# Kernel tuning notes

Measured on AMD Instinct MI355X. Metric: run time of the kernel, lower is better.

Reference implementation:

```python
import jax, jax.numpy as jnp
import numpy as np

N_DIM = 1024
N_HEAD = 16
HEAD_DIM = N_DIM // N_HEAD  # 64
HALF = HEAD_DIM // 2        # 32, per-axis RoPE dim
BASE = 10000.0


def _rope_1d(x, pos, dim_h, base=BASE):
    # x: [B,H,S,dim_h], pos: [B,H,S] int
    theta = 1.0 / (base ** (jnp.arange(0, dim_h, 2, dtype=jnp.float32) / dim_h))  # [dim_h/2]
    pos_c = jnp.maximum(pos, 0)
    ang = pos_c[..., None].astype(jnp.float32) * theta  # [B,H,S,dim_h/2]
    cos, sin = jnp.cos(ang), jnp.sin(ang)
    xs = x.astype(jnp.float32).reshape(*x.shape[:-1], dim_h // 2, 2)
    x0, x1 = xs[..., 0], xs[..., 1]
    r0 = x0 * cos - x1 * sin
    r1 = x1 * cos + x0 * sin
    m = (pos >= 0)[..., None]  # [B,H,S,1]
    r0 = jnp.where(m, r0, x0)
    r1 = jnp.where(m, r1, x1)
    out = jnp.stack([r0, r1], axis=-1).reshape(x.shape)
    return out.astype(x.dtype)


def _rope_2d(x, positions):
    # x: [B,H,S,D], positions: [B,1,S,2] -> expand over heads
    B, H, S, D = x.shape
    pos = jnp.broadcast_to(positions, (B, H, S, 2))
    xh = _rope_1d(x[..., :HALF], pos[..., 0], HALF)
    xw = _rope_1d(x[..., HALF:], pos[..., 1], HALF)
    return jnp.concatenate([xh, xw], axis=-1)


def setup_inputs() -> dict:
    key = jax.random.key(0)
    k1, k2, k3, k4 = jax.random.split(key, 4)
    B, T = 8, 1024
    x = jax.random.normal(k1, (B, T, N_DIM), dtype=jnp.float32)
    attn_mask = jnp.ones((B, 1, T), dtype=bool)
    positions = jax.random.randint(k2, (B, T, 2), 0, 1024, dtype=jnp.int64)
    s = 1.0 / np.sqrt(N_DIM)
    w_qkv = jax.random.normal(k3, (N_DIM, 3 * N_DIM), dtype=jnp.float32) * s
    w_proj = jax.random.normal(k4, (N_DIM, N_DIM), dtype=jnp.float32) * s
    return {"x": x, "attn_mask": attn_mask, "positions": positions,
            "w_qkv": w_qkv, "w_proj": w_proj}


def reference(x, attn_mask, positions, w_qkv, w_proj):
    B, T, C = x.shape
    qkv = x @ w_qkv  # [B,T,3C]
    q, k, v = jnp.split(qkv, 3, axis=2)
    # -> [B,H,T,D]
    def to_heads(t):
        return t.reshape(B, T, N_HEAD, HEAD_DIM).transpose(0, 2, 1, 3)
    q, k, v = to_heads(q), to_heads(k), to_heads(v)
    pos = positions[:, None]  # [B,1,S,2]
    q = _rope_2d(q, pos)
    k = _rope_2d(k, pos)
    scale = 1.0 / np.sqrt(HEAD_DIM)
    scores = jnp.einsum("bhsd,bhtd->bhst", q, k) * scale  # [B,H,T,T]
    mask = attn_mask[:, None]  # [B,1,1,T]
    scores = jnp.where(mask, scores, jnp.float32(-1e30))
    attn = jax.nn.softmax(scores, axis=-1)
    out = jnp.einsum("bhst,bhtd->bhsd", attn, v)  # [B,H,T,D]
    out = out.transpose(0, 2, 1, 3).reshape(B, T, C)
    y = out @ w_proj
    return y
```

## Files before the change

### kernel.cpp

```cpp
#include <hip/hip_runtime.h>
#include <math.h>

#define BATCH 8
#define TSEQ 1024
#define NDIM 1024
#define NHEAD 16
#define HDIM 64
#define QKV_COLS 3072

#define QSCALE 0.18033688011112042f
#define DEFER_THR 10.0f

#define EXP2F(x) __builtin_amdgcn_exp2f(x)

typedef __attribute__((ext_vector_type(8))) short bf16x8;
typedef __attribute__((ext_vector_type(4))) float f32x4;

__device__ inline unsigned short f2bf(float x) {
    unsigned u = __float_as_uint(x);
    unsigned r = u + 0x7fffu + ((u >> 16) & 1u);
    return (unsigned short)(r >> 16);
}
__device__ inline float bf2f(unsigned short h) {
    return __uint_as_float(((unsigned)h) << 16);
}

__device__ inline void gl16(const unsigned short* g, unsigned short* l) {
    __builtin_amdgcn_global_load_lds(
        (const __attribute__((address_space(1))) unsigned int*)g,
        (__attribute__((address_space(3))) unsigned int*)l, 16, 0, 0);
}

template<int OUT_BF16>
__global__ __launch_bounds__(256)
void gemm_bf16k(const unsigned short* __restrict__ A,
                const unsigned short* __restrict__ BT,
                void* __restrict__ Cv, int M, int N, int K) {
    __shared__ unsigned short As[128 * 32];
    __shared__ unsigned short Bs[128 * 32];
    const int tid  = threadIdx.x;
    const int wave = tid >> 6, lane = tid & 63;
    const int row0 = blockIdx.y * 128, col0 = blockIdx.x * 128;
    const int wr = (wave >> 1) * 64, wc = (wave & 1) * 64;

    f32x4 acc[4][4] = {};

    const int srow = lane >> 2;
    const int scol = (lane & 3) * 8;
    const size_t abase = (size_t)row0 * K;
    const size_t bbase = (size_t)col0 * K;
    const int i0 = wave * 2;

    for (int kt = 0; kt < K; kt += 32) {
        __syncthreads();
        gl16(&A [abase + (size_t)(i0 * 16 + srow) * K + kt + scol], &As[i0 * 512]);
        gl16(&A [abase + (size_t)((i0 + 1) * 16 + srow) * K + kt + scol], &As[(i0 + 1) * 512]);
        gl16(&BT[bbase + (size_t)(i0 * 16 + srow) * K + kt + scol], &Bs[i0 * 512]);
        gl16(&BT[bbase + (size_t)((i0 + 1) * 16 + srow) * K + kt + scol], &Bs[(i0 + 1) * 512]);
        __syncthreads();

        bf16x8 a[4], b[4];
#pragma unroll
        for (int m = 0; m < 4; ++m)
            a[m] = *(const bf16x8*)&As[(wr + m * 16 + (lane & 15)) * 32 + (lane >> 4) * 8];
#pragma unroll
        for (int n = 0; n < 4; ++n)
            b[n] = *(const bf16x8*)&Bs[(wc + n * 16 + (lane & 15)) * 32 + (lane >> 4) * 8];
#pragma unroll
        for (int m = 0; m < 4; ++m)
#pragma unroll
            for (int n = 0; n < 4; ++n)
                acc[m][n] = __builtin_amdgcn_mfma_f32_16x16x32_bf16(
                                a[m], b[n], acc[m][n], 0, 0, 0);
    }

    const int crow = row0 + wr + (lane >> 4) * 4;
    const int ccol = col0 + wc + (lane & 15);
#pragma unroll
    for (int m = 0; m < 4; ++m)
#pragma unroll
        for (int n = 0; n < 4; ++n)
#pragma unroll
            for (int j = 0; j < 4; ++j) {
                size_t idx = (size_t)(crow + m * 16 + j) * N + ccol + n * 16;
                if (OUT_BF16) ((unsigned short*)Cv)[idx] = f2bf(acc[m][n][j]);
                else          ((float*)Cv)[idx] = acc[m][n][j];
            }
}

__global__ void detect_pos(const int* __restrict__ p, int* __restrict__ flag) {
    __shared__ int s_any;
    if (threadIdx.x == 0) s_any = 0;
    __syncthreads();
    int acc = 0;
    for (int i = 1 + 2 * (int)threadIdx.x; i < BATCH * TSEQ * 2; i += 512)
        acc |= p[i];
    if (acc) atomicOr(&s_any, 1);
    __syncthreads();
    if (threadIdx.x == 0) *flag = s_any;
}

__global__ void build_tab(float2* __restrict__ tab) {
    int i = blockIdx.x * 256 + threadIdx.x;
    int pos = i >> 4, f = i & 15;
    double theta = pow(10000.0, -(double)(2 * f) / 32.0);
    double s, c;
    sincos((double)pos * theta, &s, &c);
    tab[i] = make_float2((float)c, (float)s);
}

__global__ __launch_bounds__(256)
void cvt_x(const float* __restrict__ x, unsigned short* __restrict__ xb) {
    int i = blockIdx.x * 256 + threadIdx.x;
    float4 a = *(const float4*)(x + (size_t)i * 8);
    float4 b = *(const float4*)(x + (size_t)i * 8 + 4);
    unsigned short o[8] = { f2bf(a.x), f2bf(a.y), f2bf(a.z), f2bf(a.w),
                            f2bf(b.x), f2bf(b.y), f2bf(b.z), f2bf(b.w) };
    *(uint4*)(xb + (size_t)i * 8) = *(uint4*)o;
}

__global__ __launch_bounds__(256)
void transpose_w(const float* __restrict__ W, unsigned short* __restrict__ WT,
                 int K, int N) {
    __shared__ float Ls[16][68];
    const int n0 = blockIdx.x * 64, k0 = blockIdx.y * 16;
    const int t = threadIdx.x;
    {
        int kr = t >> 6, nn = t & 63;
#pragma unroll
        for (int j = 0; j < 4; ++j)
            Ls[kr * 4 + j][nn] = W[(size_t)(k0 + kr * 4 + j) * N + n0 + nn];
    }
    __syncthreads();
    {
        int r = t >> 2, c = (t & 3) * 4;
        unsigned short o[4];
#pragma unroll
        for (int j = 0; j < 4; ++j) o[j] = f2bf(Ls[c + j][r]);
        *(uint2*)&WT[(size_t)(n0 + r) * K + k0 + c] = *(uint2*)o;
    }
}

__global__ __launch_bounds__(256)
void rope_bf16(unsigned short* __restrict__ qkv,
               const int* __restrict__ positions,
               const int* __restrict__ flag,
               const float2* __restrict__ tab) {
    int g = blockIdx.x * 256 + threadIdx.x;
    int row = g >> 10, p = g & 1023;
    int tensor = p >> 9;
    int rr   = p & 511;
    int head = rr >> 5, pi = rr & 31;
    int half = pi >> 4, i = pi & 15;

    int stride = (*flag) ? 1 : 2;
    int pos = positions[(row * 2 + half) * stride];

    unsigned short* ptr = qkv + (size_t)row * QKV_COLS + tensor * NDIM +
                          head * HDIM + half * 32 + i * 2;
    unsigned pair = *(unsigned*)ptr;
    float x0 = bf2f((unsigned short)(pair & 0xffff));
    float x1 = bf2f((unsigned short)(pair >> 16));
    float c = 1.f, s = 0.f;
    if (pos >= 0) {
        float2 cs = tab[(pos < 1024 ? pos : 1023) * 16 + i];
        c = cs.x; s = cs.y;
    }
    float r0 = x0 * c - x1 * s;
    float r1 = x1 * c + x0 * s;
    if (tensor == 0) { r0 *= QSCALE; r1 *= QSCALE; }
    unsigned outp = (unsigned)f2bf(r0) | ((unsigned)f2bf(r1) << 16);
    *(unsigned*)ptr = outp;
}

__global__ __launch_bounds__(256)
void vtrans(const unsigned short* __restrict__ qkvb,
            unsigned short* __restrict__ VT) {
    __shared__ unsigned short Ls[64][72];
    const int blk = blockIdx.x;
    const int bh = blk >> 4, t0 = (blk & 15) * 64;
    const int b = bh >> 4, h = bh & 15;
    const int tid = threadIdx.x;
    {
        int r = tid >> 2, p4 = (tid & 3) * 16;
        const uint4* g = (const uint4*)(qkvb +
            (size_t)(b * TSEQ + t0 + r) * QKV_COLS + 2 * NDIM + h * HDIM + p4);
        uint4 v0 = g[0], v1 = g[1];
        *(uint4*)&Ls[r][p4] = v0;
        *(uint4*)&Ls[r][p4 + 8] = v1;
    }
    __syncthreads();
    {
        int d = tid >> 2, tc = tid & 3;
        unsigned short o[16];
#pragma unroll
        for (int j = 0; j < 16; ++j) o[j] = Ls[tc * 16 + j][d];
        unsigned short* dst = VT + ((size_t)bh * 64 + d) * TSEQ + t0 + tc * 16;
        *(uint4*)dst = *(uint4*)o;
        *(uint4*)(dst + 8) = *(uint4*)(o + 8);
    }
}

__device__ __forceinline__ void attn_tile(
    const unsigned short* KB, const unsigned short* VB,
    unsigned short* PsW,
    const bf16x8& qf0, const bf16x8& qf1,
    f32x4 (&Oacc)[4], float& m, float& l, int lo, int hi)
{
    f32x4 s[4] = {};
    __builtin_amdgcn_s_setprio(1);
#pragma unroll
    for (int n = 0; n < 4; ++n) {
        int R = n * 16 + lo, sw = R & 7;
        bf16x8 k0 = *(const bf16x8*)&KB[R * 64 + ((hi ^ sw) << 3)];
        bf16x8 k1 = *(const bf16x8*)&KB[R * 64 + (((hi + 4) ^ sw) << 3)];
        s[n] = __builtin_amdgcn_mfma_f32_16x16x32_bf16(k0, qf0, s[n], 0, 0, 0);
        s[n] = __builtin_amdgcn_mfma_f32_16x16x32_bf16(k1, qf1, s[n], 0, 0, 0);
    }
    __builtin_amdgcn_s_setprio(0);

    float a0 = fmaxf(fmaxf(s[0][0], s[0][1]), s[0][2]);
    float a1 = fmaxf(fmaxf(s[0][3], s[1][0]), s[1][1]);
    float a2 = fmaxf(fmaxf(s[1][2], s[1][3]), s[2][0]);
    float a3 = fmaxf(fmaxf(s[2][1], s[2][2]), s[2][3]);
    float a4 = fmaxf(fmaxf(s[3][0], s[3][1]), s[3][2]);
    float b0 = fmaxf(fmaxf(a0, a1), a2);
    float b1 = fmaxf(fmaxf(a3, a4), s[3][3]);
    float pmax = fmaxf(b0, b1);
    pmax = fmaxf(pmax, __shfl_xor(pmax, 16));
    pmax = fmaxf(pmax, __shfl_xor(pmax, 32));

    if (!__all(pmax <= m + DEFER_THR)) {
        float mnew  = fmaxf(m, pmax);
        float alpha = EXP2F(m - mnew);
        l *= alpha;
        m = mnew;
#pragma unroll
        for (int j = 0; j < 4; ++j) {
            float aj = __shfl(alpha, 4 * hi + j);
#pragma unroll
            for (int n = 0; n < 4; ++n) Oacc[n][j] *= aj;
        }
    }

    float rsum = 0.f;
#pragma unroll
    for (int n = 0; n < 4; ++n)
#pragma unroll
        for (int j = 0; j < 4; ++j) {
            float p = EXP2F(s[n][j] - m);
            s[n][j] = p;
            rsum += p;
        }
    rsum += __shfl_xor(rsum, 16);
    rsum += __shfl_xor(rsum, 32);
    l += rsum;

#pragma unroll
    for (int n = 0; n < 4; ++n) {
        unsigned d0, d1;
        asm("v_cvt_pk_bf16_f32 %0, %1, %2" : "=v"(d0) : "v"(s[n][0]), "v"(s[n][1]));
        asm("v_cvt_pk_bf16_f32 %0, %1, %2" : "=v"(d1) : "v"(s[n][2]), "v"(s[n][3]));
        *(uint2*)&PsW[lo * 72 + 16 * n + 4 * hi] = make_uint2(d0, d1);
    }
    bf16x8 pa0 = *(const bf16x8*)&PsW[lo * 72 + 8 * hi];
    bf16x8 pa1 = *(const bf16x8*)&PsW[lo * 72 + 32 + 8 * hi];

    __builtin_amdgcn_s_setprio(1);
#pragma unroll
    for (int n = 0; n < 4; ++n) {
        int R = n * 16 + lo, sw = R & 7;
        bf16x8 v0 = *(const bf16x8*)&VB[R * 64 + ((hi ^ sw) << 3)];
        bf16x8 v1 = *(const bf16x8*)&VB[R * 64 + (((hi + 4) ^ sw) << 3)];
        Oacc[n] = __builtin_amdgcn_mfma_f32_16x16x32_bf16(pa0, v0, Oacc[n], 0, 0, 0);
        Oacc[n] = __builtin_amdgcn_mfma_f32_16x16x32_bf16(pa1, v1, Oacc[n], 0, 0, 0);
    }
    __builtin_amdgcn_s_setprio(0);
}

__global__ __launch_bounds__(512)
void attn_mfma4(const unsigned short* __restrict__ qkvb,
                const unsigned short* __restrict__ VT,
                unsigned short* __restrict__ out) {
    __shared__ unsigned short Kl[2][64 * 64];
    __shared__ unsigned short Vl[2][64 * 64];
    __shared__ unsigned short Ps[8][16][72];

    const int bh = blockIdx.x;
    const int b = bh >> 4, h = bh & 15;
    const int q0 = blockIdx.y * 128;
    const int tid = threadIdx.x, wave = tid >> 6, lane = tid & 63;
    const int lo = lane & 15, hi = lane >> 4;

    const size_t qrow_base = (size_t)b * TSEQ * QKV_COLS + h * HDIM;
    const unsigned short* Kg = qkvb + qrow_base + NDIM;
    const unsigned short* Vg = VT + (size_t)bh * HDIM * TSEQ;

    const int srow   = tid >> 3;
    const int schunk = tid & 7;
    const int sc     = (schunk ^ (srow & 7)) * 8;
    const unsigned short* kg0 = Kg + (size_t)srow * QKV_COLS + sc;
    const unsigned short* vg0 = Vg + (size_t)srow * TSEQ + sc;
    unsigned short* const kd0 = &Kl[0][(wave * 8) * 64];
    unsigned short* const kd1 = &Kl[1][(wave * 8) * 64];
    unsigned short* const vd0 = &Vl[0][(wave * 8) * 64];
    unsigned short* const vd1 = &Vl[1][(wave * 8) * 64];
    unsigned short* const PsW = &Ps[wave][0][0];

    bf16x8 qf0, qf1;
    {
        const unsigned short* qp =
            qkvb + qrow_base + (size_t)(q0 + wave * 16 + lo) * QKV_COLS;
        qf0 = *(const bf16x8*)(qp + hi * 8);
        qf1 = *(const bf16x8*)(qp + 32 + hi * 8);
    }

    gl16(kg0, kd0);
    gl16(vg0, vd0);
    __syncthreads();

    f32x4 Oacc[4] = {};
    float m = -1e30f;
    float l = 0.f;

    for (int kt = 0; kt < 16; kt += 2) {
        gl16(kg0 + (size_t)(kt + 1) * 64 * QKV_COLS, kd1);
        gl16(vg0 + (size_t)(kt + 1) * 64, vd1);
        attn_tile(Kl[0], Vl[0], PsW, qf0, qf1, Oacc, m, l, lo, hi);
        __syncthreads();

        if (kt < 14) {
            gl16(kg0 + (size_t)(kt + 2) * 64 * QKV_COLS, kd0);
            gl16(vg0 + (size_t)(kt + 2) * 64, vd0);
        }
        attn_tile(Kl[1], Vl[1], PsW, qf0, qf1, Oacc, m, l, lo, hi);
        __syncthreads();
    }

#pragma unroll
    for (int j = 0; j < 4; ++j) {
        float inv = 1.f / __shfl(l, 4 * hi + j);
        int r = b * TSEQ + q0 + wave * 16 + 4 * hi + j;
#pragma unroll
        for (int n = 0; n < 4; ++n)
            out[(size_t)r * NDIM + h * HDIM + n * 16 + lo] =
                f2bf(Oacc[n][j] * inv);
    }
}

extern "C" void kernel_launch(void* const* d_in, const int* in_sizes, int n_in,
                              void* d_out, int out_size, void* d_ws, size_t ws_size,
                              hipStream_t stream) {
    (void)in_sizes; (void)n_in; (void)out_size; (void)ws_size;

    const float* x         = (const float*)d_in[0];
    const int*   positions = (const int*)d_in[2];
    const float* w_qkv     = (const float*)d_in[3];
    const float* w_proj    = (const float*)d_in[4];
    float* y = (float*)d_out;

    char* ws = (char*)d_ws;
    unsigned short* qkvb   = (unsigned short*)(ws);
    unsigned short* VT     = (unsigned short*)(ws + 50331648);
    unsigned short* aout   = (unsigned short*)(ws + 67108864);
    unsigned short* xb     = (unsigned short*)(ws + 83886080);
    unsigned short* wqkvT  = (unsigned short*)(ws + 100663296);
    unsigned short* wprojT = (unsigned short*)(ws + 106954752);
    float2*         tab    = (float2*)(ws + 109051904);
    int*            flag   = (int*)(ws + 109182976);

    detect_pos<<<1, 256, 0, stream>>>(positions, flag);
    build_tab<<<64, 256, 0, stream>>>(tab);
    cvt_x<<<(BATCH * TSEQ * NDIM / 8) / 256, 256, 0, stream>>>(x, xb);
    transpose_w<<<dim3(QKV_COLS / 64, NDIM / 16), 256, 0, stream>>>(w_qkv, wqkvT, NDIM, QKV_COLS);
    transpose_w<<<dim3(NDIM / 64, NDIM / 16), 256, 0, stream>>>(w_proj, wprojT, NDIM, NDIM);

    gemm_bf16k<1><<<dim3(QKV_COLS / 128, BATCH * TSEQ / 128), 256, 0, stream>>>(
        xb, wqkvT, qkvb, BATCH * TSEQ, QKV_COLS, NDIM);

    rope_bf16<<<(BATCH * TSEQ * 1024) / 256, 256, 0, stream>>>(qkvb, positions, flag, tab);

    vtrans<<<BATCH * NHEAD * (TSEQ / 64), 256, 0, stream>>>(qkvb, VT);

    attn_mfma4<<<dim3(BATCH * NHEAD, TSEQ / 128), 512, 0, stream>>>(qkvb, VT, aout);

    gemm_bf16k<0><<<dim3(NDIM / 128, BATCH * TSEQ / 128), 256, 0, stream>>>(
        aout, wprojT, y, BATCH * TSEQ, NDIM, NDIM);
}
```

Before: 208.7 us.

## Pipeline GEMM with 4-stage async LDS buffering, swizzled LDS and block remap

Replaces the single-buffered bf16 GEMM with a 4-stage ring of LDS buffers, filled by async global-to-LDS loads issued three K-steps ahead and gated by vmcnt waits and barriers. The LDS layout is XOR-swizzled to cut bank conflicts. Blocks are remapped across 8 groups so neighbouring blocks share tiles in cache. MFMA sections get raised wave priority. The goal is to hide global load latency behind the MFMA work. In exchange K is hardcoded to 1024, and the larger LDS footprint may limit occupancy.

```diff
diff --git a/kernel.cpp b/kernel.cpp
--- a/kernel.cpp
+++ b/kernel.cpp
@@ -31,48 +31,87 @@
         (__attribute__((address_space(3))) unsigned int*)l, 16, 0, 0);
 }
 
+#define WAITVM(n) asm volatile("s_waitcnt vmcnt(" #n ")" ::: "memory")
+
 template<int OUT_BF16>
-__global__ __launch_bounds__(256)
-void gemm_bf16k(const unsigned short* __restrict__ A,
-                const unsigned short* __restrict__ BT,
-                void* __restrict__ Cv, int M, int N, int K) {
-    __shared__ unsigned short As[128 * 32];
-    __shared__ unsigned short Bs[128 * 32];
-    const int tid  = threadIdx.x;
-    const int wave = tid >> 6, lane = tid & 63;
-    const int row0 = blockIdx.y * 128, col0 = blockIdx.x * 128;
+__global__ __launch_bounds__(256, 2)
+void gemm_pipe(const unsigned short* __restrict__ A,
+               const unsigned short* __restrict__ BT,
+               void* __restrict__ Cv, int N, int nx, int cpx) {
+    __shared__ unsigned short lds[4][8192];
+
+    const int tid = threadIdx.x, wave = tid >> 6, lane = tid & 63;
+    const int lo = lane & 15, hi = lane >> 4;
     const int wr = (wave >> 1) * 64, wc = (wave & 1) * 64;
 
+    const int bid = blockIdx.x;
+    const int swz = (bid & 7) * cpx + (bid >> 3);
+    const int ty = swz / nx, tx = swz - ty * nx;
+    const int row0 = ty * 128, col0 = tx * 128;
+
+    const int brow = lane >> 3;
+    const int sc   = (lane & 7) ^ brow;
+    const unsigned short* gs[4];
+#pragma unroll
+    for (int i = 0; i < 4; ++i) {
+        int r = (wave * 4 + i) * 8 + brow;
+        gs[i] = (sc < 4) ? A  + (size_t)(row0 + r) * 1024 + sc * 8
+                         : BT + (size_t)(col0 + r) * 1024 + (sc - 4) * 8;
+    }
+
+    const int swA = (hi ^ (lo & 7)) * 8;
+    const int swB = ((hi + 4) ^ (lo & 7)) * 8;
+
     f32x4 acc[4][4] = {};
 
-    const int srow = lane >> 2;
-    const int scol = (lane & 3) * 8;
-    const size_t abase = (size_t)row0 * K;
-    const size_t bbase = (size_t)col0 * K;
-    const int i0 = wave * 2;
-
-    for (int kt = 0; kt < K; kt += 32) {
-        __syncthreads();
-        gl16(&A [abase + (size_t)(i0 * 16 + srow) * K + kt + scol], &As[i0 * 512]);
-        gl16(&A [abase + (size_t)((i0 + 1) * 16 + srow) * K + kt + scol], &As[(i0 + 1) * 512]);
-        gl16(&BT[bbase + (size_t)(i0 * 16 + srow) * K + kt + scol], &Bs[i0 * 512]);
-        gl16(&BT[bbase + (size_t)((i0 + 1) * 16 + srow) * K + kt + scol], &Bs[(i0 + 1) * 512]);
-        __syncthreads();
-
-        bf16x8 a[4], b[4];
-#pragma unroll
-        for (int m = 0; m < 4; ++m)
-            a[m] = *(const bf16x8*)&As[(wr + m * 16 + (lane & 15)) * 32 + (lane >> 4) * 8];
-#pragma unroll
-        for (int n = 0; n < 4; ++n)
-            b[n] = *(const bf16x8*)&Bs[(wc + n * 16 + (lane & 15)) * 32 + (lane >> 4) * 8];
-#pragma unroll
-        for (int m = 0; m < 4; ++m)
-#pragma unroll
-            for (int n = 0; n < 4; ++n)
-                acc[m][n] = __builtin_amdgcn_mfma_f32_16x16x32_bf16(
-                                a[m], b[n], acc[m][n], 0, 0, 0);
-    }
+#pragma unroll
+    for (int p = 0; p < 3; ++p)
+#pragma unroll
+        for (int i = 0; i < 4; ++i)
+            gl16(gs[i] + (size_t)p * 32, &lds[p][(wave * 4 + i) * 512]);
+
+#define GSTEP(S_, VM_, t_, issue_)                                            \
+    {                                                                         \
+        if (issue_) {                                                         \
+            _Pragma("unroll")                                                 \
+            for (int i = 0; i < 4; ++i)                                       \
+                gl16(gs[i] + (size_t)((t_) + 3) * 32,                         \
+                     &lds[((S_) + 3) & 3][(wave * 4 + i) * 512]);             \
+        }                                                                     \
+        WAITVM(VM_);                                                          \
+        __builtin_amdgcn_s_barrier();                                         \
+        asm volatile("" ::: "memory");                                        \
+        bf16x8 a[4], b[4];                                                    \
+        _Pragma("unroll")                                                     \
+        for (int m = 0; m < 4; ++m)                                           \
+            a[m] = *(const bf16x8*)&lds[S_][(wr + m * 16 + lo) * 64 + swA];   \
+        _Pragma("unroll")                                                     \
+        for (int n = 0; n < 4; ++n)                                           \
+            b[n] = *(const bf16x8*)&lds[S_][(wc + n * 16 + lo) * 64 + swB];   \
+        __builtin_amdgcn_s_setprio(1);                                        \
+        _Pragma("unroll")                                                     \
+        for (int m = 0; m < 4; ++m)                                           \
+            _Pragma("unroll")                                                 \
+            for (int n = 0; n < 4; ++n)                                       \
+                acc[m][n] = __builtin_amdgcn_mfma_f32_16x16x32_bf16(          \
+                    a[m], b[n], acc[m][n], 0, 0, 0);                          \
+        __builtin_amdgcn_s_setprio(0);                                        \
+        __builtin_amdgcn_s_barrier();                                         \
+        asm volatile("" ::: "memory");                                        \
+    }
+
+    for (int to = 0; to < 7; ++to) {
+        const int t = to * 4;
+        GSTEP(0, 12, t + 0, true);
+        GSTEP(1, 12, t + 1, true);
+        GSTEP(2, 12, t + 2, true);
+        GSTEP(3, 12, t + 3, true);
+    }
+    GSTEP(0, 12, 28, true);
+    GSTEP(1, 8,  29, false);
+    GSTEP(2, 4,  30, false);
+    GSTEP(3, 0,  31, false);
+#undef GSTEP
 
     const int crow = row0 + wr + (lane >> 4) * 4;
     const int ccol = col0 + wc + (lane & 15);
@@ -375,8 +414,7 @@
     transpose_w<<<dim3(QKV_COLS / 64, NDIM / 16), 256, 0, stream>>>(w_qkv, wqkvT, NDIM, QKV_COLS);
     transpose_w<<<dim3(NDIM / 64, NDIM / 16), 256, 0, stream>>>(w_proj, wprojT, NDIM, NDIM);
 
-    gemm_bf16k<1><<<dim3(QKV_COLS / 128, BATCH * TSEQ / 128), 256, 0, stream>>>(
-        xb, wqkvT, qkvb, BATCH * TSEQ, QKV_COLS, NDIM);
+    gemm_pipe<1><<<1536, 256, 0, stream>>>(xb, wqkvT, qkvb, QKV_COLS, 24, 192);
 
     rope_bf16<<<(BATCH * TSEQ * 1024) / 256, 256, 0, stream>>>(qkvb, positions, flag, tab);
 
@@ -384,6 +422,5 @@
 
     attn_mfma4<<<dim3(BATCH * NHEAD, TSEQ / 128), 512, 0, stream>>>(qkvb, VT, aout);
 
-    gemm_bf16k<0><<<dim3(NDIM / 128, BATCH * TSEQ / 128), 256, 0, stream>>>(
-        aout, wprojT, y, BATCH * TSEQ, NDIM, NDIM);
-}
+    gemm_pipe<0><<<512, 256, 0, stream>>>(aout, wprojT, y, NDIM, 8, 64);
+}
```

Result: faster. 194.3 us (-6.9%).
